# Kernel optimization log

Measured on AMD Instinct MI355X. Metric: run time of the kernel, lower is better.

Reference implementation:

```python
import jax, jax.numpy as jnp
import numpy as np

N, M, D_IN, H1, D, OUT_C = 2048, 128, 352, 512, 256, 13


def _lin_bn_relu(x, w, b, g, be):
    # 1x1 conv == linear over last dim; BN (eval) folded to per-channel affine (g, be)
    return jax.nn.relu(g * (x @ w.T + b) + be)


def _encode(x, wA, bA, gA, beA, wB, bB, gB, beB):
    return _lin_bn_relu(_lin_bn_relu(x, wA, bA, gA, beA), wB, bB, gB, beB)


def setup_inputs() -> dict:
    key = jax.random.key(0)
    ks = iter(jax.random.split(key, 64))

    def wgt(shape, s=0.05):
        return (jax.random.normal(next(ks), shape, jnp.float32) * s)

    def gamma(c):
        return 1.0 + 0.05 * jax.random.normal(next(ks), (c,), jnp.float32)

    inp = {}
    inp['ext_fea'] = jax.random.normal(next(ks), (N, D_IN), jnp.float32)
    inp['lab_fea'] = jax.random.normal(next(ks), (M, D_IN), jnp.float32)
    # convs1: 352->512->256, each Conv1d(1x1)+BN+ReLU
    inp.update(w1a=wgt((H1, D_IN)), b1a=wgt((H1,)), g1a=gamma(H1), be1a=wgt((H1,)))
    inp.update(w1b=wgt((D, H1)), b1b=wgt((D,)), g1b=gamma(D), be1b=wgt((D,)))
    # convs2: same shapes
    inp.update(w2a=wgt((H1, D_IN)), b2a=wgt((H1,)), g2a=gamma(H1), be2a=wgt((H1,)))
    inp.update(w2b=wgt((D, H1)), b2b=wgt((D,)), g2b=gamma(D), be2b=wgt((D,)))
    # wei_conv SharedMLP [256,32,64,256]: three Conv2d(1x1)+BN+ReLU
    inp.update(mw1=wgt((32, D)), mb1=wgt((32,)), mg1=gamma(32), mbe1=wgt((32,)))
    inp.update(mw2=wgt((64, 32)), mb2=wgt((64,)), mg2=gamma(64), mbe2=wgt((64,)))
    inp.update(mw3=wgt((D, 64)), mb3=wgt((D,)), mg3=gamma(D), mbe3=wgt((D,)))
    # fc
    inp.update(fcw=wgt((OUT_C, D)), fcb=wgt((OUT_C,)))
    return inp


def reference(ext_fea, lab_fea,
              w1a, b1a, g1a, be1a, w1b, b1b, g1b, be1b,
              w2a, b2a, g2a, be2a, w2b, b2b, g2b, be2b,
              mw1, mb1, mg1, mbe1, mw2, mb2, mg2, mbe2, mw3, mb3, mg3, mbe3,
              fcw, fcb):
    A = _encode(ext_fea, w1a, b1a, g1a, be1a, w1b, b1b, g1b, be1b)   # [N, 256]
    B = _encode(lab_fea, w2a, b2a, g2a, be2a, w2b, b2b, g2b, be2b)   # [M, 256]
    diff = A[:, None, :] - B[None, :, :]                             # [N, M, 256]
    h = _lin_bn_relu(diff, mw1, mb1, mg1, mbe1)                      # [N, M, 32]
    h = _lin_bn_relu(h, mw2, mb2, mg2, mbe2)                         # [N, M, 64]
    wei = _lin_bn_relu(h, mw3, mb3, mg3, mbe3)                       # [N, M, 256]
    # torch softmax over dim=-1 of [1,256,N,M] == over M == axis 1 here
    wei = jax.nn.softmax(wei, axis=1)
    att = jnp.sum(wei * diff, axis=1)                                # [N, 256]
    return att @ fcw.T + fcb                                         # [N, 13]
```

## Files before the change

### kernel.cpp

```cpp
#include <hip/hip_runtime.h>
#include <stdint.h>


typedef __attribute__((ext_vector_type(4))) float float4_t;
typedef __attribute__((ext_vector_type(4))) float f32x4;
typedef __attribute__((ext_vector_type(8))) short bf16x8;
typedef __attribute__((ext_vector_type(8))) unsigned short ushort8_t;
typedef unsigned short ushort_t;

__device__ __forceinline__ unsigned short f2b(float f) {
  union { float f; unsigned int i; } v; v.f = f;
  unsigned int x = v.i;
  return (unsigned short)((x + 0x7FFFu + ((x >> 16) & 1u)) >> 16);
}

template<int ISBF>
__device__ __forceinline__ ushort8_t ld8(const void* base, size_t idx) {
  if constexpr (ISBF) {
    return *(const ushort8_t*)((const ushort_t*)base + idx);
  } else {
    const float* p = (const float*)base + idx;
    float4_t v0 = *(const float4_t*)p;
    float4_t v1 = *(const float4_t*)(p + 4);
    ushort8_t u;
    #pragma unroll
    for (int e = 0; e < 4; ++e) { u[e] = f2b(v0[e]); u[4 + e] = f2b(v1[e]); }
    return u;
  }
}

template<int XBF, int WBF, int OUT_BF16>
__global__ __launch_bounds__(256) void enc_mfma(
    const void* __restrict__ XA, const void* __restrict__ WA,
    const float* __restrict__ bA, const float* __restrict__ gA, const float* __restrict__ beA,
    void* __restrict__ YA,
    const void* __restrict__ XB, const void* __restrict__ WB,
    const float* __restrict__ bB, const float* __restrict__ gB, const float* __restrict__ beB,
    void* __restrict__ YB, float* __restrict__ YBT,
    int J, int K, int nbxA)
{
  __shared__ ushort_t Xs[2][32][40];
  __shared__ ushort_t Ws[2][32][40];
  const int bx = blockIdx.x, by = blockIdx.y;
  const void* X; const void* W;
  const float *bb, *gg, *bev; void* Y; int i0, isB;
  if (bx < nbxA) { X = XA; W = WA; bb = bA; gg = gA; bev = beA; Y = YA; i0 = bx * 32; isB = 0; }
  else           { X = XB; W = WB; bb = bB; gg = gB; bev = beB; Y = YB; i0 = (bx - nbxA) * 32; isB = 1; }
  const int j0 = by * 32;
  const int tid = threadIdx.x, w = tid >> 6, lane = tid & 63, lg = lane >> 4, lr = lane & 15;
  const int mt = w >> 1, ct = w & 1;
  const int row = tid >> 2, k8 = (tid & 3) * 8;

  f32x4 acc = f32x4{0.f, 0.f, 0.f, 0.f};

  ushort8_t sv = (row < 32) ? ld8<XBF>(X, (size_t)(i0 + row) * K + k8)
                            : ld8<WBF>(W, (size_t)(j0 + row - 32) * K + k8);
  for (int kt = 0; kt < K; kt += 32) {
    const int buf = (kt >> 5) & 1;
    if (row < 32) *(ushort8_t*)&Xs[buf][row][k8] = sv;
    else          *(ushort8_t*)&Ws[buf][row - 32][k8] = sv;
    __syncthreads();
    if (kt + 32 < K)
      sv = (row < 32) ? ld8<XBF>(X, (size_t)(i0 + row) * K + kt + 32 + k8)
                      : ld8<WBF>(W, (size_t)(j0 + row - 32) * K + kt + 32 + k8);
    bf16x8 af = *(const bf16x8*)&Xs[buf][mt * 16 + lr][lg * 8];
    bf16x8 bf_ = *(const bf16x8*)&Ws[buf][ct * 16 + lr][lg * 8];
    acc = __builtin_amdgcn_mfma_f32_16x16x32_bf16(af, bf_, acc, 0, 0, 0);
  }
  const int c = j0 + ct * 16 + lr;
  const float g = gg[c], bv = bb[c], ev = bev[c];
  #pragma unroll
  for (int r = 0; r < 4; ++r) {
    const int rowo = i0 + mt * 16 + 4 * lg + r;
    float t = fmaxf(g * (acc[r] + bv) + ev, 0.f);
    if (OUT_BF16) ((ushort_t*)Y)[(size_t)rowo * J + c] = f2b(t);
    else {
      ((float*)Y)[(size_t)rowo * J + c] = t;
      if (isB && YBT) YBT[(size_t)c * 128 + rowo] = t;
    }
  }
}

__global__ __launch_bounds__(256) void proj32(
    const float* __restrict__ Aenc, const float* __restrict__ Benc,
    const float* __restrict__ mw1, const float* __restrict__ mb1,
    const float* __restrict__ mg1, const float* __restrict__ mbe1,
    float* __restrict__ PA2, float* __restrict__ PB2, int nbxA,
    const float* __restrict__ mw2, const float* __restrict__ mw3,
    ushort_t* __restrict__ mw2b, ushort_t* __restrict__ mw3b)
{
  __shared__ float ps[4][32];
  const int tid = threadIdx.x, bx = blockIdx.x;
  if (bx >= nbxA + 32) {
    const int g = (bx - nbxA - 32) * 256 + tid;
    const float* s; ushort_t* d; int j;
    if (g < 256) { s = mw2; d = mw2b; j = g; }
    else         { s = mw3; d = mw3b; j = g - 256; }
    float4_t v0 = *(const float4_t*)&s[(size_t)j * 8];
    float4_t v1 = *(const float4_t*)&s[(size_t)j * 8 + 4];
    ushort8_t u;
    #pragma unroll
    for (int e = 0; e < 4; ++e) { u[e] = f2b(v0[e]); u[4 + e] = f2b(v1[e]); }
    *(ushort8_t*)&d[(size_t)j * 8] = u;
    return;
  }
  const float* X; float* P; int n0, wb;
  if (bx < nbxA) { X = Aenc; P = PA2; n0 = bx * 4; wb = 1; }
  else           { X = Benc; P = PB2; n0 = (bx - nbxA) * 4; wb = 0; }
  const int k = tid & 31, r = (tid >> 5) & 3, half = tid >> 7;
  const int n = n0 + r;
  const float* xp = &X[(size_t)n * 256 + half * 128];
  const float* wp = &mw1[k * 256 + half * 128];
  float s = 0.f;
  #pragma unroll 8
  for (int q = 0; q < 128; q += 4) {
    float4_t xv = *(const float4_t*)&xp[q];
    float4_t wv = *(const float4_t*)&wp[q];
    #pragma unroll
    for (int e = 0; e < 4; ++e) s = fmaf(xv[e], wv[e], s);
  }
  if (half == 1) ps[r][k] = s;
  __syncthreads();
  if (half == 0) {
    s += ps[r][k];
    P[(size_t)n * 32 + k] = wb ? (mg1[k] * (s + mb1[k]) + mbe1[k]) : (mg1[k] * s);
  }
}

__global__ __launch_bounds__(512, 2) void main_attn(
    const float* __restrict__ PA2, const float* __restrict__ PB2,
    const float* __restrict__ A, const float* __restrict__ BmT,
    const ushort_t* __restrict__ mw2b, const float* __restrict__ mb2,
    const float* __restrict__ mg2, const float* __restrict__ mbe2,
    const ushort_t* __restrict__ mw3b, const float* __restrict__ mb3,
    const float* __restrict__ mg3, const float* __restrict__ mbe3,
    const float* __restrict__ fcw, const float* __restrict__ fcb,
    float* __restrict__ outp)
{
  __shared__ __align__(16) char smem[42240];
  float* attLs = (float*)(smem + 36864);
  float* part  = (float*)(smem + 38912);

  const int tid = threadIdx.x;
  const int w = tid >> 6, lane = tid & 63, lg = lane >> 4, lr = lane & 15;
  const int n0 = blockIdx.x * 2;
  const float LOG2E = 1.4426950408889634f;

  float g2h[4], b2h[4], e2h[4];
  #pragma unroll
  for (int jt = 0; jt < 4; ++jt) {
    const int j = jt * 16 + lr;
    g2h[jt] = mg2[j]; b2h[jt] = mb2[j]; e2h[jt] = mbe2[j];
  }
  float gs3[2], cs3[2];
  #pragma unroll
  for (int ct = 0; ct < 2; ++ct) {
    const int c = w * 32 + ct * 16 + lr;
    const float g = mg3[c];
    gs3[ct] = g * LOG2E;
    cs3[ct] = (g * mb3[c] + mbe3[c]) * LOG2E;
  }

  #pragma unroll
  for (int nn = 0; nn < 2; ++nn) {
    const int n = n0 + nn;
    ushort_t* h2s = (ushort_t*)(smem + nn * 18432);

    {
      f32x4 acc1[4];
      #pragma unroll
      for (int jt = 0; jt < 4; ++jt) acc1[jt] = f32x4{0.f, 0.f, 0.f, 0.f};
      bf16x8 a1, b1[4];
      {
        const float* pa = &PA2[(size_t)n * 32 + lg * 8];
        float4_t pa0 = *(const float4_t*)pa;
        float4_t pa1 = *(const float4_t*)(pa + 4);
        const int m = w * 16 + lr;
        const float* pb = &PB2[(size_t)m * 32 + lg * 8];
        float4_t pb0 = *(const float4_t*)pb;
        float4_t pb1 = *(const float4_t*)(pb + 4);
        bf16x8 u;
        #pragma unroll
        for (int e = 0; e < 4; ++e) {
          u[e]     = (short)f2b(fmaxf(pa0[e] - pb0[e], 0.f));
          u[4 + e] = (short)f2b(fmaxf(pa1[e] - pb1[e], 0.f));
        }
        a1 = u;
      }
      #pragma unroll
      for (int jt = 0; jt < 4; ++jt)
        b1[jt] = *(const bf16x8*)&mw2b[(jt * 16 + lr) * 32 + lg * 8];
      #pragma unroll
      for (int jt = 0; jt < 4; ++jt)
        acc1[jt] = __builtin_amdgcn_mfma_f32_16x16x32_bf16(a1, b1[jt], acc1[jt], 0, 0, 0);
      #pragma unroll
      for (int jt = 0; jt < 4; ++jt)
        #pragma unroll
        for (int r = 0; r < 4; ++r)
          h2s[(w * 16 + 4 * lg + r) * 72 + jt * 16 + lr] =
              f2b(fmaxf(g2h[jt] * (acc1[jt][r] + b2h[jt]) + e2h[jt], 0.f));
    }
    __syncthreads();

    f32x4 acc[8][2];
    #pragma unroll
    for (int mt = 0; mt < 8; ++mt) {
      acc[mt][0] = f32x4{0.f, 0.f, 0.f, 0.f};
      acc[mt][1] = f32x4{0.f, 0.f, 0.f, 0.f};
    }
    #pragma unroll
    for (int ks = 0; ks < 2; ++ks) {
      bf16x8 bfr[2];
      #pragma unroll
      for (int q = 0; q < 2; ++q) {
        const int c = w * 32 + q * 16 + lr;
        bfr[q] = *(const bf16x8*)&mw3b[(size_t)c * 64 + ks * 32 + lg * 8];
      }
      #pragma unroll
      for (int mt = 0; mt < 8; ++mt) {
        bf16x8 af = *(const bf16x8*)&h2s[(mt * 16 + lr) * 72 + ks * 32 + lg * 8];
        acc[mt][0] = __builtin_amdgcn_mfma_f32_16x16x32_bf16(af, bfr[0], acc[mt][0], 0, 0, 0);
        acc[mt][1] = __builtin_amdgcn_mfma_f32_16x16x32_bf16(af, bfr[1], acc[mt][1], 0, 0, 0);
      }
    }

    float smv[2], wbv[2];
    #pragma unroll
    for (int q = 0; q < 2; ++q) {
      const int c = w * 32 + q * 16 + lr;
      f32x4 sm4 = f32x4{0.f, 0.f, 0.f, 0.f};
      f32x4 wb4 = f32x4{0.f, 0.f, 0.f, 0.f};
      #pragma unroll
      for (int mt = 0; mt < 8; ++mt) {
        float4_t bv4 = *(const float4_t*)&BmT[(size_t)c * 128 + mt * 16 + 4 * lg];
        #pragma unroll
        for (int r = 0; r < 4; ++r) {
          float t = fmaf(gs3[q], acc[mt][q][r], cs3[q]);
          float p = __builtin_amdgcn_exp2f(__builtin_amdgcn_fmed3f(t, 0.f, 80.f));
          sm4[r] += p;
          wb4[r] = fmaf(p, bv4[r], wb4[r]);
        }
      }
      smv[q] = (sm4[0] + sm4[1]) + (sm4[2] + sm4[3]);
      wbv[q] = (wb4[0] + wb4[1]) + (wb4[2] + wb4[3]);
    }
    #pragma unroll
    for (int st = 16; st <= 32; st <<= 1) {
      #pragma unroll
      for (int q = 0; q < 2; ++q) {
        smv[q] += __shfl_xor(smv[q], st, 64);
        wbv[q] += __shfl_xor(wbv[q], st, 64);
      }
    }
    if (lg == 0) {
      #pragma unroll
      for (int q = 0; q < 2; ++q) {
        const int c = w * 32 + q * 16 + lr;
        attLs[nn * 256 + c] = A[(size_t)n * 256 + c] - wbv[q] / smv[q];
      }
    }
  }
  __syncthreads();

  {
    const int o = tid >> 5, gp = tid & 31;
    if (o < 13) {
      float4_t wv[2];
      #pragma unroll
      for (int i = 0; i < 2; ++i)
        wv[i] = *(const float4_t*)&fcw[(size_t)o * 256 + gp * 8 + i * 4];
      #pragma unroll
      for (int nn = 0; nn < 2; ++nn) {
        float s = 0.f;
        #pragma unroll
        for (int i = 0; i < 2; ++i) {
          float4_t av = *(const float4_t*)&attLs[nn * 256 + gp * 8 + i * 4];
          #pragma unroll
          for (int e = 0; e < 4; ++e) s = fmaf(av[e], wv[i][e], s);
        }
        part[nn * 416 + o * 32 + gp] = s;
      }
    }
  }
  __syncthreads();
  if (tid < 26) {
    const int nn = tid / 13, o = tid % 13;
    float s = fcb[o];
    #pragma unroll
    for (int gp = 0; gp < 32; ++gp) s += part[nn * 416 + o * 32 + gp];
    outp[(size_t)(n0 + nn) * 13 + o] = s;
  }
}

extern "C" void kernel_launch(void* const* d_in, const int* in_sizes, int n_in,
                              void* d_out, int out_size, void* d_ws, size_t ws_size,
                              hipStream_t stream)
{
  const float* ext = (const float*)d_in[0];
  const float* lab = (const float*)d_in[1];
  const float* w1a = (const float*)d_in[2];
  const float* b1a = (const float*)d_in[3];
  const float* g1a = (const float*)d_in[4];
  const float* be1a= (const float*)d_in[5];
  const float* w1b = (const float*)d_in[6];
  const float* b1b = (const float*)d_in[7];
  const float* g1b = (const float*)d_in[8];
  const float* be1b= (const float*)d_in[9];
  const float* w2a = (const float*)d_in[10];
  const float* b2a = (const float*)d_in[11];
  const float* g2a = (const float*)d_in[12];
  const float* be2a= (const float*)d_in[13];
  const float* w2b = (const float*)d_in[14];
  const float* b2b = (const float*)d_in[15];
  const float* g2b = (const float*)d_in[16];
  const float* be2b= (const float*)d_in[17];
  const float* mw1 = (const float*)d_in[18];
  const float* mb1 = (const float*)d_in[19];
  const float* mg1 = (const float*)d_in[20];
  const float* mbe1= (const float*)d_in[21];
  const float* mw2 = (const float*)d_in[22];
  const float* mb2 = (const float*)d_in[23];
  const float* mg2 = (const float*)d_in[24];
  const float* mbe2= (const float*)d_in[25];
  const float* mw3 = (const float*)d_in[26];
  const float* mb3 = (const float*)d_in[27];
  const float* mg3 = (const float*)d_in[28];
  const float* mbe3= (const float*)d_in[29];
  const float* fcw = (const float*)d_in[30];
  const float* fcb = (const float*)d_in[31];

  char* ws = (char*)d_ws;
  ushort_t* Y1ab = (ushort_t*)(ws);
  float*    PA2  = (float*)(ws);
  float*    PB2  = (float*)(ws + 262144);
  float*    Aenc = (float*)(ws + (2u << 20));
  char* b5 = ws + (4u << 20);
  ushort_t* mw2b = (ushort_t*)(b5);
  ushort_t* mw3b = (ushort_t*)(b5 + 4096);
  ushort_t* Y1bb = (ushort_t*)(b5 + 36864);
  float*    Benc = (float*)(b5 + 167936);
  float*    BencT= (float*)(b5 + 299008);

  enc_mfma<0, 0, 1><<<dim3(68, 16), 256, 0, stream>>>(
      (const void*)ext, (const void*)w1a, b1a, g1a, be1a, (void*)Y1ab,
      (const void*)lab, (const void*)w2a, b2a, g2a, be2a, (void*)Y1bb,
      (float*)nullptr, 512, 352, 64);
  enc_mfma<1, 0, 0><<<dim3(68, 8), 256, 0, stream>>>(
      (const void*)Y1ab, (const void*)w1b, b1b, g1b, be1b, (void*)Aenc,
      (const void*)Y1bb, (const void*)w2b, b2b, g2b, be2b, (void*)Benc,
      BencT, 256, 512, 64);
  proj32<<<553, 256, 0, stream>>>(Aenc, Benc, mw1, mb1, mg1, mbe1, PA2, PB2, 512,
                                  mw2, mw3, mw2b, mw3b);
  main_attn<<<1024, 512, 0, stream>>>(PA2, PB2, Aenc, BencT,
                                      mw2b, mb2, mg2, mbe2, mw3b, mb3, mg3, mbe3,
                                      fcw, fcb, (float*)d_out);
}
```

Baseline: 95.07 us.

## Assign one query row per wavefront in attention kernel, removing block syncs

The main attention kernel now gives each wavefront its own output row n. That wave computes the full 128x64 h2 tile into private LDS, loops over all 256 channels in 16-column chunks, and finishes the fc projection with wave shuffles. This removes the block-wide __syncthreads and the cross-wave split of the channel dimension. It also cuts the grid from 1024 blocks of 512 threads to 512 blocks of 256 threads. In exchange each wave redoes the mw2 MFMA work over all m and reloads mw3 fragments for every row, and LDS per block rises to about 76 KB, which may limit occupancy.

```diff
diff --git a/kernel.cpp b/kernel.cpp
--- a/kernel.cpp
+++ b/kernel.cpp
@@ -127,7 +127,7 @@
   }
 }
 
-__global__ __launch_bounds__(512, 2) void main_attn(
+__global__ __launch_bounds__(256, 2) void main_attn(
     const float* __restrict__ PA2, const float* __restrict__ PB2,
     const float* __restrict__ A, const float* __restrict__ BmT,
     const ushort_t* __restrict__ mw2b, const float* __restrict__ mb2,
@@ -137,59 +137,41 @@
     const float* __restrict__ fcw, const float* __restrict__ fcb,
     float* __restrict__ outp)
 {
-  __shared__ __align__(16) char smem[42240];
-  float* attLs = (float*)(smem + 36864);
-  float* part  = (float*)(smem + 38912);
-
+  __shared__ __align__(16) char smem[77824];
   const int tid = threadIdx.x;
   const int w = tid >> 6, lane = tid & 63, lg = lane >> 4, lr = lane & 15;
-  const int n0 = blockIdx.x * 2;
+  const int n = blockIdx.x * 4 + w;
+  ushort_t* h2s = (ushort_t*)(smem + w * 19456);
+  float* attL   = (float*)(smem + w * 19456 + 18432);
   const float LOG2E = 1.4426950408889634f;
 
-  float g2h[4], b2h[4], e2h[4];
-  #pragma unroll
-  for (int jt = 0; jt < 4; ++jt) {
-    const int j = jt * 16 + lr;
-    g2h[jt] = mg2[j]; b2h[jt] = mb2[j]; e2h[jt] = mbe2[j];
-  }
-  float gs3[2], cs3[2];
-  #pragma unroll
-  for (int ct = 0; ct < 2; ++ct) {
-    const int c = w * 32 + ct * 16 + lr;
-    const float g = mg3[c];
-    gs3[ct] = g * LOG2E;
-    cs3[ct] = (g * mb3[c] + mbe3[c]) * LOG2E;
-  }
-
-  #pragma unroll
-  for (int nn = 0; nn < 2; ++nn) {
-    const int n = n0 + nn;
-    ushort_t* h2s = (ushort_t*)(smem + nn * 18432);
-
-    {
+  {
+    bf16x8 b1[4];
+    float g2h[4], b2h[4], e2h[4];
+    #pragma unroll
+    for (int jt = 0; jt < 4; ++jt) {
+      b1[jt] = *(const bf16x8*)&mw2b[(jt * 16 + lr) * 32 + lg * 8];
+      const int j = jt * 16 + lr;
+      g2h[jt] = mg2[j]; b2h[jt] = mb2[j]; e2h[jt] = mbe2[j];
+    }
+    const float* pa = &PA2[(size_t)n * 32 + lg * 8];
+    float4_t pa0 = *(const float4_t*)pa;
+    float4_t pa1 = *(const float4_t*)(pa + 4);
+    #pragma unroll
+    for (int mt = 0; mt < 8; ++mt) {
+      const int m = mt * 16 + lr;
+      const float* pb = &PB2[(size_t)m * 32 + lg * 8];
+      float4_t pb0 = *(const float4_t*)pb;
+      float4_t pb1 = *(const float4_t*)(pb + 4);
+      bf16x8 a1;
+      #pragma unroll
+      for (int e = 0; e < 4; ++e) {
+        a1[e]     = (short)f2b(fmaxf(pa0[e] - pb0[e], 0.f));
+        a1[4 + e] = (short)f2b(fmaxf(pa1[e] - pb1[e], 0.f));
+      }
       f32x4 acc1[4];
       #pragma unroll
       for (int jt = 0; jt < 4; ++jt) acc1[jt] = f32x4{0.f, 0.f, 0.f, 0.f};
-      bf16x8 a1, b1[4];
-      {
-        const float* pa = &PA2[(size_t)n * 32 + lg * 8];
-        float4_t pa0 = *(const float4_t*)pa;
-        float4_t pa1 = *(const float4_t*)(pa + 4);
-        const int m = w * 16 + lr;
-        const float* pb = &PB2[(size_t)m * 32 + lg * 8];
-        float4_t pb0 = *(const float4_t*)pb;
-        float4_t pb1 = *(const float4_t*)(pb + 4);
-        bf16x8 u;
-        #pragma unroll
-        for (int e = 0; e < 4; ++e) {
-          u[e]     = (short)f2b(fmaxf(pa0[e] - pb0[e], 0.f));
-          u[4 + e] = (short)f2b(fmaxf(pa1[e] - pb1[e], 0.f));
-        }
-        a1 = u;
-      }
-      #pragma unroll
-      for (int jt = 0; jt < 4; ++jt)
-        b1[jt] = *(const bf16x8*)&mw2b[(jt * 16 + lr) * 32 + lg * 8];
       #pragma unroll
       for (int jt = 0; jt < 4; ++jt)
         acc1[jt] = __builtin_amdgcn_mfma_f32_16x16x32_bf16(a1, b1[jt], acc1[jt], 0, 0, 0);
@@ -197,98 +179,63 @@
       for (int jt = 0; jt < 4; ++jt)
         #pragma unroll
         for (int r = 0; r < 4; ++r)
-          h2s[(w * 16 + 4 * lg + r) * 72 + jt * 16 + lr] =
+          h2s[(mt * 16 + 4 * lg + r) * 72 + jt * 16 + lr] =
               f2b(fmaxf(g2h[jt] * (acc1[jt][r] + b2h[jt]) + e2h[jt], 0.f));
     }
-    __syncthreads();
-
-    f32x4 acc[8][2];
+  }
+
+  #pragma unroll 2
+  for (int ct = 0; ct < 16; ++ct) {
+    const int c = ct * 16 + lr;
+    bf16x8 bfr0 = *(const bf16x8*)&mw3b[(size_t)c * 64 + lg * 8];
+    bf16x8 bfr1 = *(const bf16x8*)&mw3b[(size_t)c * 64 + 32 + lg * 8];
+    f32x4 acc[8];
+    #pragma unroll
+    for (int mt = 0; mt < 8; ++mt) acc[mt] = f32x4{0.f, 0.f, 0.f, 0.f};
     #pragma unroll
     for (int mt = 0; mt < 8; ++mt) {
-      acc[mt][0] = f32x4{0.f, 0.f, 0.f, 0.f};
-      acc[mt][1] = f32x4{0.f, 0.f, 0.f, 0.f};
-    }
-    #pragma unroll
-    for (int ks = 0; ks < 2; ++ks) {
-      bf16x8 bfr[2];
-      #pragma unroll
-      for (int q = 0; q < 2; ++q) {
-        const int c = w * 32 + q * 16 + lr;
-        bfr[q] = *(const bf16x8*)&mw3b[(size_t)c * 64 + ks * 32 + lg * 8];
+      bf16x8 af0 = *(const bf16x8*)&h2s[(mt * 16 + lr) * 72 + lg * 8];
+      acc[mt] = __builtin_amdgcn_mfma_f32_16x16x32_bf16(af0, bfr0, acc[mt], 0, 0, 0);
+      bf16x8 af1 = *(const bf16x8*)&h2s[(mt * 16 + lr) * 72 + 32 + lg * 8];
+      acc[mt] = __builtin_amdgcn_mfma_f32_16x16x32_bf16(af1, bfr1, acc[mt], 0, 0, 0);
+    }
+    const float g = mg3[c];
+    const float gs = g * LOG2E;
+    const float cs = (g * mb3[c] + mbe3[c]) * LOG2E;
+    f32x4 sm4 = f32x4{0.f, 0.f, 0.f, 0.f};
+    f32x4 wb4 = f32x4{0.f, 0.f, 0.f, 0.f};
+    #pragma unroll
+    for (int mt = 0; mt < 8; ++mt) {
+      float4_t bv4 = *(const float4_t*)&BmT[(size_t)c * 128 + mt * 16 + 4 * lg];
+      #pragma unroll
+      for (int r = 0; r < 4; ++r) {
+        float t = fmaf(gs, acc[mt][r], cs);
+        float p = __builtin_amdgcn_exp2f(__builtin_amdgcn_fmed3f(t, 0.f, 80.f));
+        sm4[r] += p;
+        wb4[r] = fmaf(p, bv4[r], wb4[r]);
       }
-      #pragma unroll
-      for (int mt = 0; mt < 8; ++mt) {
-        bf16x8 af = *(const bf16x8*)&h2s[(mt * 16 + lr) * 72 + ks * 32 + lg * 8];
-        acc[mt][0] = __builtin_amdgcn_mfma_f32_16x16x32_bf16(af, bfr[0], acc[mt][0], 0, 0, 0);
-        acc[mt][1] = __builtin_amdgcn_mfma_f32_16x16x32_bf16(af, bfr[1], acc[mt][1], 0, 0, 0);
-      }
-    }
-
-    float smv[2], wbv[2];
-    #pragma unroll
-    for (int q = 0; q < 2; ++q) {
-      const int c = w * 32 + q * 16 + lr;
-      f32x4 sm4 = f32x4{0.f, 0.f, 0.f, 0.f};
-      f32x4 wb4 = f32x4{0.f, 0.f, 0.f, 0.f};
-      #pragma unroll
-      for (int mt = 0; mt < 8; ++mt) {
-        float4_t bv4 = *(const float4_t*)&BmT[(size_t)c * 128 + mt * 16 + 4 * lg];
-        #pragma unroll
-        for (int r = 0; r < 4; ++r) {
-          float t = fmaf(gs3[q], acc[mt][q][r], cs3[q]);
-          float p = __builtin_amdgcn_exp2f(__builtin_amdgcn_fmed3f(t, 0.f, 80.f));
-          sm4[r] += p;
-          wb4[r] = fmaf(p, bv4[r], wb4[r]);
-        }
-      }
-      smv[q] = (sm4[0] + sm4[1]) + (sm4[2] + sm4[3]);
-      wbv[q] = (wb4[0] + wb4[1]) + (wb4[2] + wb4[3]);
-    }
-    #pragma unroll
-    for (int st = 16; st <= 32; st <<= 1) {
-      #pragma unroll
-      for (int q = 0; q < 2; ++q) {
-        smv[q] += __shfl_xor(smv[q], st, 64);
-        wbv[q] += __shfl_xor(wbv[q], st, 64);
-      }
-    }
-    if (lg == 0) {
-      #pragma unroll
-      for (int q = 0; q < 2; ++q) {
-        const int c = w * 32 + q * 16 + lr;
-        attLs[nn * 256 + c] = A[(size_t)n * 256 + c] - wbv[q] / smv[q];
-      }
-    }
-  }
-  __syncthreads();
+    }
+    float sm = (sm4[0] + sm4[1]) + (sm4[2] + sm4[3]);
+    float wb = (wb4[0] + wb4[1]) + (wb4[2] + wb4[3]);
+    sm += __shfl_xor(sm, 16, 64);  wb += __shfl_xor(wb, 16, 64);
+    sm += __shfl_xor(sm, 32, 64);  wb += __shfl_xor(wb, 32, 64);
+    if (lg == 0)
+      attL[c] = A[(size_t)n * 256 + c] - wb / sm;
+  }
 
   {
-    const int o = tid >> 5, gp = tid & 31;
-    if (o < 13) {
-      float4_t wv[2];
-      #pragma unroll
-      for (int i = 0; i < 2; ++i)
-        wv[i] = *(const float4_t*)&fcw[(size_t)o * 256 + gp * 8 + i * 4];
-      #pragma unroll
-      for (int nn = 0; nn < 2; ++nn) {
-        float s = 0.f;
-        #pragma unroll
-        for (int i = 0; i < 2; ++i) {
-          float4_t av = *(const float4_t*)&attLs[nn * 256 + gp * 8 + i * 4];
-          #pragma unroll
-          for (int e = 0; e < 4; ++e) s = fmaf(av[e], wv[i][e], s);
-        }
-        part[nn * 416 + o * 32 + gp] = s;
-      }
-    }
-  }
-  __syncthreads();
-  if (tid < 26) {
-    const int nn = tid / 13, o = tid % 13;
-    float s = fcb[o];
-    #pragma unroll
-    for (int gp = 0; gp < 32; ++gp) s += part[nn * 416 + o * 32 + gp];
-    outp[(size_t)(n0 + nn) * 13 + o] = s;
+    float4_t av = *(const float4_t*)&attL[lane * 4];
+    #pragma unroll
+    for (int o = 0; o < 13; ++o) {
+      float4_t wv = *(const float4_t*)&fcw[(size_t)o * 256 + lane * 4];
+      float s = av[0] * wv[0];
+      s = fmaf(av[1], wv[1], s);
+      s = fmaf(av[2], wv[2], s);
+      s = fmaf(av[3], wv[3], s);
+      #pragma unroll
+      for (int st = 1; st <= 32; st <<= 1) s += __shfl_xor(s, st, 64);
+      if (lane == 0) outp[(size_t)n * 13 + o] = s + fcb[o];
+    }
   }
 }
 
@@ -351,7 +298,7 @@
       BencT, 256, 512, 64);
   proj32<<<553, 256, 0, stream>>>(Aenc, Benc, mw1, mb1, mg1, mbe1, PA2, PB2, 512,
                                   mw2, mw3, mw2b, mw3b);
-  main_attn<<<1024, 512, 0, stream>>>(PA2, PB2, Aenc, BencT,
-                                      mw2b, mb2, mg2, mbe2, mw3b, mb3, mg3, mbe3,
-                                      fcw, fcb, (float*)d_out);
-}
+  main_attn<<<512, 256, 0, stream>>>(PA2, PB2, Aenc, BencT,
+                                     mw2b, mb2, mg2, mbe2, mw3b, mb3, mg3, mbe3,
+                                     fcw, fcb, (float*)d_out);
+}
```

Measured after the change: 86.34 us. 1.1x faster.
